# Performance work log

Hardware: AMD Instinct MI355X
Metric: run time of the kernel (lower is better)

## Reference

```python
import jax, jax.numpy as jnp
import numpy as np

B, C = 32, 32768
ENC_DIM, VOCAB, TOK_DIM, HIDDEN = 1024, 100000, 256, 512


def setup_inputs() -> dict:
    key = jax.random.key(0)
    k1, k2, k3, k4, k5 = jax.random.split(key, 5)
    enc_vec = jax.random.normal(k1, (B, ENC_DIM), dtype=jnp.float32)
    cand_tok = jax.random.randint(k2, (B, C), 0, VOCAB, dtype=jnp.int64)
    tok_emb = jax.random.normal(k3, (VOCAB, TOK_DIM), dtype=jnp.float32) * 0.02
    # PAD (0) and BOS (1) rows fixed to zeros, as in __init__
    tok_emb = tok_emb.at[0].set(0.0).at[1].set(0.0)
    W1 = jax.random.normal(k4, (HIDDEN, ENC_DIM), dtype=jnp.float32) * 0.02
    b1 = jnp.zeros((HIDDEN,), dtype=jnp.float32)
    W2 = jax.random.normal(k5, (TOK_DIM, HIDDEN), dtype=jnp.float32) * 0.02
    return {"enc_vec": enc_vec, "cand_tok": cand_tok, "tok_emb": tok_emb,
            "W1": W1, "b1": b1, "W2": W2}


def reference(enc_vec, cand_tok, tok_emb, W1, b1, W2):
    # q_proj: Linear -> GELU (exact, torch default) -> (Dropout inactive at eval) -> Linear (no bias)
    h = jax.nn.gelu(enc_vec @ W1.T + b1, approximate=False)  # (B, hidden)
    q = h @ W2.T                                             # (B, tok_dim)
    Wc = tok_emb[cand_tok]                                   # (B, C, tok_dim) gather
    logits = jnp.einsum('be,bce->bc', q, Wc)                 # (B, C)
    return logits
```

## Files before the change

kernel.cpp:

```cpp
#include <hip/hip_runtime.h>
#include <math.h>

#define B_    32
#define C_    32768
#define ENC_  1024
#define VOCAB_ 100000
#define TOK_  256
#define HID_  512

typedef __attribute__((ext_vector_type(8))) short short8;
typedef __attribute__((ext_vector_type(4))) float f32x4;

__device__ __forceinline__ float gelu_exact(float x) {
    return 0.5f * x * (1.0f + erff(x * 0.70710678118654752f));
}

__device__ __forceinline__ unsigned short f2bf(float f) {
    unsigned u = __builtin_bit_cast(unsigned, f);
    return (unsigned short)((u + 0x7fffu + ((u >> 16) & 1u)) >> 16);
}

__device__ __forceinline__ short8 pack8(float4 a, float4 b) {
    short8 r;
    r[0] = (short)f2bf(a.x); r[1] = (short)f2bf(a.y);
    r[2] = (short)f2bf(a.z); r[3] = (short)f2bf(a.w);
    r[4] = (short)f2bf(b.x); r[5] = (short)f2bf(b.y);
    r[6] = (short)f2bf(b.z); r[7] = (short)f2bf(b.w);
    return r;
}

__global__ __launch_bounds__(256) void k1_hidden(
    const float* __restrict__ enc, const float* __restrict__ W1,
    const float* __restrict__ b1, float* __restrict__ h)
{
    __shared__ float enc_lds[ENC_];
    const int b = blockIdx.y;
    const int tid = threadIdx.x;
    ((float4*)enc_lds)[tid] = ((const float4*)(enc + b * ENC_))[tid];
    __syncthreads();

    const int hw = tid >> 5, lane = tid & 31;
    const int jbase = blockIdx.x * 64 + hw * 8;
    const float4* enc4 = (const float4*)enc_lds;
    #pragma unroll
    for (int i = 0; i < 8; ++i) {
        const int j = jbase + i;
        const float4* wrow = (const float4*)(W1 + (size_t)j * ENC_);
        float acc = 0.f;
        #pragma unroll
        for (int t = 0; t < 8; ++t) {
            const int k4 = t * 32 + lane;
            float4 w = wrow[k4];
            float4 e = enc4[k4];
            acc += w.x * e.x + w.y * e.y + w.z * e.z + w.w * e.w;
        }
        #pragma unroll
        for (int m = 16; m >= 1; m >>= 1) acc += __shfl_xor(acc, m, 32);
        if (lane == 0) h[b * HID_ + j] = gelu_exact(acc + b1[j]);
    }
}

__global__ __launch_bounds__(256) void k2_q(
    const float* __restrict__ h, const float* __restrict__ W2,
    float* __restrict__ q)
{
    __shared__ float h_lds[HID_];
    const int b = blockIdx.y;
    const int tid = threadIdx.x;
    ((float2*)h_lds)[tid] = ((const float2*)(h + b * HID_))[tid];
    __syncthreads();

    const int hw = tid >> 5, lane = tid & 31;
    const int jbase = blockIdx.x * 64 + hw * 8;
    const float4* h4 = (const float4*)h_lds;
    #pragma unroll
    for (int i = 0; i < 8; ++i) {
        const int j = jbase + i;
        const float4* wrow = (const float4*)(W2 + (size_t)j * HID_);
        float acc = 0.f;
        #pragma unroll
        for (int t = 0; t < 4; ++t) {
            const int k4 = t * 32 + lane;
            float4 w = wrow[k4];
            float4 e = h4[k4];
            acc += w.x * e.x + w.y * e.y + w.z * e.z + w.w * e.w;
        }
        #pragma unroll
        for (int m = 16; m >= 1; m >>= 1) acc += __shfl_xor(acc, m, 32);
        if (lane == 0) q[b * TOK_ + j] = acc;
    }
}

__global__ __launch_bounds__(256) void k3_qall_mfma(
    const float* __restrict__ q, const float* __restrict__ tok_emb,
    float* __restrict__ q_all)
{
    __shared__ short8 q_lds[1024];
    const int tid  = threadIdx.x;
    const int lane = tid & 63;
    const int hw   = tid >> 6;
    const int m  = lane & 15;
    const int kq = lane >> 4;

    #pragma unroll
    for (int ks2 = 0; ks2 < 2; ++ks2) {
        const int ks = hw * 2 + ks2;
        #pragma unroll
        for (int n = 0; n < 2; ++n) {
            const float4* p = (const float4*)(q + (n * 16 + m) * TOK_ + ks * 32 + kq * 8);
            q_lds[(ks * 2 + n) * 64 + lane] = pack8(p[0], p[1]);
        }
    }
    __syncthreads();

    const int wave = blockIdx.x * 4 + hw;
    if (wave >= VOCAB_ / 32) return;
    const int v0 = wave * 32;

    const float* abase = tok_emb + (size_t)(v0 + m) * TOK_ + kq * 8;

    float4 st[2][4];
    #pragma unroll
    for (int t = 0; t < 2; ++t) {
        st[0][t * 2 + 0] = *(const float4*)(abase + t * 16 * TOK_);
        st[0][t * 2 + 1] = *(const float4*)(abase + t * 16 * TOK_ + 4);
    }

    f32x4 acc[2][2] = {{{0.f,0.f,0.f,0.f},{0.f,0.f,0.f,0.f}},
                       {{0.f,0.f,0.f,0.f},{0.f,0.f,0.f,0.f}}};
    #pragma unroll
    for (int ks = 0; ks < 8; ++ks) {
        const int cur = ks & 1, nxt = cur ^ 1;
        if (ks < 7) {
            #pragma unroll
            for (int t = 0; t < 2; ++t) {
                st[nxt][t * 2 + 0] = *(const float4*)(abase + t * 16 * TOK_ + (ks + 1) * 32);
                st[nxt][t * 2 + 1] = *(const float4*)(abase + t * 16 * TOK_ + (ks + 1) * 32 + 4);
            }
        }
        short8 b0 = q_lds[(ks * 2 + 0) * 64 + lane];
        short8 b1 = q_lds[(ks * 2 + 1) * 64 + lane];
        #pragma unroll
        for (int t = 0; t < 2; ++t) {
            short8 af = pack8(st[cur][t * 2 + 0], st[cur][t * 2 + 1]);
            acc[t][0] = __builtin_amdgcn_mfma_f32_16x16x32_bf16(af, b0, acc[t][0], 0, 0, 0);
            acc[t][1] = __builtin_amdgcn_mfma_f32_16x16x32_bf16(af, b1, acc[t][1], 0, 0, 0);
        }
    }

    #pragma unroll
    for (int t = 0; t < 2; ++t) {
        #pragma unroll
        for (int n = 0; n < 2; ++n) {
            float4 r;
            r.x = acc[t][n][0]; r.y = acc[t][n][1];
            r.z = acc[t][n][2]; r.w = acc[t][n][3];
            float* dst = q_all + (size_t)(n * 16 + m) * VOCAB_ + v0 + t * 16 + kq * 4;
            *(float4*)dst = r;
        }
    }
}

__global__ __launch_bounds__(256) void k4_gather(
    const int* __restrict__ cand, const float* __restrict__ q_all,
    float* __restrict__ out)
{
    const int b     = blockIdx.x & 31;
    const int chunk = blockIdx.x >> 5;
    const int c0 = chunk * 1024 + threadIdx.x * 4;
    const int4 t = *(const int4*)(cand + (size_t)b * C_ + c0);
    const float* row = q_all + (size_t)b * VOCAB_;
    float4 r;
    r.x = row[t.x];
    r.y = row[t.y];
    r.z = row[t.z];
    r.w = row[t.w];
    *(float4*)(out + (size_t)b * C_ + c0) = r;
}

extern "C" void kernel_launch(void* const* d_in, const int* in_sizes, int n_in,
                              void* d_out, int out_size, void* d_ws, size_t ws_size,
                              hipStream_t stream) {
    const float* enc     = (const float*)d_in[0];
    const int*   cand    = (const int*)  d_in[1];
    const float* tok_emb = (const float*)d_in[2];
    const float* W1      = (const float*)d_in[3];
    const float* b1      = (const float*)d_in[4];
    const float* W2      = (const float*)d_in[5];
    float* out = (float*)d_out;

    float* h     = (float*)d_ws;
    float* q     = h + B_ * HID_;
    float* q_all = q + B_ * TOK_;

    k1_hidden<<<dim3(8, 32), 256, 0, stream>>>(enc, W1, b1, h);
    k2_q     <<<dim3(4, 32), 256, 0, stream>>>(h, W2, q);

    const int tiles = VOCAB_ / 32;
    k3_qall_mfma<<<(tiles + 3) / 4, 256, 0, stream>>>(q, tok_emb, q_all);

    k4_gather<<<32 * 32, 256, 0, stream>>>(cand, q_all, out);
}
```

Before: 198.3 us.

## Store q_all as bf16 and use persistent atomic-counter tile scheduling

The q_all intermediate is now written and read as bf16, halving the traffic for the scatter-like store and the random gather. The MFMA kernel becomes a persistent grid of 512 blocks, where each wave grabs vocab tiles from a global atomic counter that is reset with a memset. This cuts the q_all footprint and its cache pressure, at the cost of an extra memset launch, per-tile atomics, and bf16 rounding on the output logits.

```diff
diff --git a/kernel.cpp b/kernel.cpp
--- a/kernel.cpp
+++ b/kernel.cpp
@@ -1,4 +1,5 @@
 #include <hip/hip_runtime.h>
+#include <hip/hip_bf16.h>
 #include <math.h>
 
 #define B_    32
@@ -7,6 +8,7 @@
 #define VOCAB_ 100000
 #define TOK_  256
 #define HID_  512
+#define TILES_ (VOCAB_ / 32)
 
 typedef __attribute__((ext_vector_type(8))) short short8;
 typedef __attribute__((ext_vector_type(4))) float f32x4;
@@ -93,7 +95,7 @@
 
 __global__ __launch_bounds__(256) void k3_qall_mfma(
     const float* __restrict__ q, const float* __restrict__ tok_emb,
-    float* __restrict__ q_all)
+    __hip_bfloat16* __restrict__ q_all, int* __restrict__ counter)
 {
     __shared__ short8 q_lds[1024];
     const int tid  = threadIdx.x;
@@ -113,68 +115,72 @@
     }
     __syncthreads();
 
-    const int wave = blockIdx.x * 4 + hw;
-    if (wave >= VOCAB_ / 32) return;
-    const int v0 = wave * 32;
-
-    const float* abase = tok_emb + (size_t)(v0 + m) * TOK_ + kq * 8;
-
-    float4 st[2][4];
-    #pragma unroll
-    for (int t = 0; t < 2; ++t) {
-        st[0][t * 2 + 0] = *(const float4*)(abase + t * 16 * TOK_);
-        st[0][t * 2 + 1] = *(const float4*)(abase + t * 16 * TOK_ + 4);
-    }
-
-    f32x4 acc[2][2] = {{{0.f,0.f,0.f,0.f},{0.f,0.f,0.f,0.f}},
-                       {{0.f,0.f,0.f,0.f},{0.f,0.f,0.f,0.f}}};
-    #pragma unroll
-    for (int ks = 0; ks < 8; ++ks) {
-        const int cur = ks & 1, nxt = cur ^ 1;
-        if (ks < 7) {
+    for (;;) {
+        int tile;
+        if (lane == 0) tile = atomicAdd(counter, 1);
+        tile = __builtin_amdgcn_readfirstlane(tile);
+        if (tile >= TILES_) break;
+        const int v0 = tile * 32;
+
+        const float* abase = tok_emb + (size_t)(v0 + m) * TOK_ + kq * 8;
+
+        float4 st[2][4];
+        #pragma unroll
+        for (int t = 0; t < 2; ++t) {
+            st[0][t * 2 + 0] = *(const float4*)(abase + t * 16 * TOK_);
+            st[0][t * 2 + 1] = *(const float4*)(abase + t * 16 * TOK_ + 4);
+        }
+
+        f32x4 acc[2][2] = {{{0.f,0.f,0.f,0.f},{0.f,0.f,0.f,0.f}},
+                           {{0.f,0.f,0.f,0.f},{0.f,0.f,0.f,0.f}}};
+        #pragma unroll
+        for (int ks = 0; ks < 8; ++ks) {
+            const int cur = ks & 1, nxt = cur ^ 1;
+            if (ks < 7) {
+                #pragma unroll
+                for (int t = 0; t < 2; ++t) {
+                    st[nxt][t * 2 + 0] = *(const float4*)(abase + t * 16 * TOK_ + (ks + 1) * 32);
+                    st[nxt][t * 2 + 1] = *(const float4*)(abase + t * 16 * TOK_ + (ks + 1) * 32 + 4);
+                }
+            }
+            short8 b0 = q_lds[(ks * 2 + 0) * 64 + lane];
+            short8 b1 = q_lds[(ks * 2 + 1) * 64 + lane];
             #pragma unroll
             for (int t = 0; t < 2; ++t) {
-                st[nxt][t * 2 + 0] = *(const float4*)(abase + t * 16 * TOK_ + (ks + 1) * 32);
-                st[nxt][t * 2 + 1] = *(const float4*)(abase + t * 16 * TOK_ + (ks + 1) * 32 + 4);
+                short8 af = pack8(st[cur][t * 2 + 0], st[cur][t * 2 + 1]);
+                acc[t][0] = __builtin_amdgcn_mfma_f32_16x16x32_bf16(af, b0, acc[t][0], 0, 0, 0);
+                acc[t][1] = __builtin_amdgcn_mfma_f32_16x16x32_bf16(af, b1, acc[t][1], 0, 0, 0);
             }
         }
-        short8 b0 = q_lds[(ks * 2 + 0) * 64 + lane];
-        short8 b1 = q_lds[(ks * 2 + 1) * 64 + lane];
+
         #pragma unroll
         for (int t = 0; t < 2; ++t) {
-            short8 af = pack8(st[cur][t * 2 + 0], st[cur][t * 2 + 1]);
-            acc[t][0] = __builtin_amdgcn_mfma_f32_16x16x32_bf16(af, b0, acc[t][0], 0, 0, 0);
-            acc[t][1] = __builtin_amdgcn_mfma_f32_16x16x32_bf16(af, b1, acc[t][1], 0, 0, 0);
-        }
-    }
-
-    #pragma unroll
-    for (int t = 0; t < 2; ++t) {
-        #pragma unroll
-        for (int n = 0; n < 2; ++n) {
-            float4 r;
-            r.x = acc[t][n][0]; r.y = acc[t][n][1];
-            r.z = acc[t][n][2]; r.w = acc[t][n][3];
-            float* dst = q_all + (size_t)(n * 16 + m) * VOCAB_ + v0 + t * 16 + kq * 4;
-            *(float4*)dst = r;
+            #pragma unroll
+            for (int n = 0; n < 2; ++n) {
+                ushort4 r;
+                r.x = f2bf(acc[t][n][0]); r.y = f2bf(acc[t][n][1]);
+                r.z = f2bf(acc[t][n][2]); r.w = f2bf(acc[t][n][3]);
+                __hip_bfloat16* dst = q_all + (size_t)(n * 16 + m) * VOCAB_ + v0 + t * 16 + kq * 4;
+                *(ushort4*)dst = r;
+            }
         }
     }
 }
 
 __global__ __launch_bounds__(256) void k4_gather(
-    const int* __restrict__ cand, const float* __restrict__ q_all,
+    const int* __restrict__ cand, const __hip_bfloat16* __restrict__ q_all,
     float* __restrict__ out)
 {
     const int b     = blockIdx.x & 31;
     const int chunk = blockIdx.x >> 5;
     const int c0 = chunk * 1024 + threadIdx.x * 4;
     const int4 t = *(const int4*)(cand + (size_t)b * C_ + c0);
-    const float* row = q_all + (size_t)b * VOCAB_;
+    const __hip_bfloat16* row = q_all + (size_t)b * VOCAB_;
     float4 r;
-    r.x = row[t.x];
-    r.y = row[t.y];
-    r.z = row[t.z];
-    r.w = row[t.w];
+    r.x = __bfloat162float(row[t.x]);
+    r.y = __bfloat162float(row[t.y]);
+    r.z = __bfloat162float(row[t.z]);
+    r.w = __bfloat162float(row[t.w]);
     *(float4*)(out + (size_t)b * C_ + c0) = r;
 }
 
@@ -189,15 +195,15 @@
     const float* W2      = (const float*)d_in[5];
     float* out = (float*)d_out;
 
-    float* h     = (float*)d_ws;
-    float* q     = h + B_ * HID_;
-    float* q_all = q + B_ * TOK_;
+    float* h = (float*)d_ws;
+    float* q = h + B_ * HID_;
+    __hip_bfloat16* q_all = (__hip_bfloat16*)(q + B_ * TOK_);
+    int* counter = (int*)((char*)(q_all + (size_t)B_ * VOCAB_) + 256);
+
+    hipMemsetAsync(counter, 0, sizeof(int), stream);
 
     k1_hidden<<<dim3(8, 32), 256, 0, stream>>>(enc, W1, b1, h);
     k2_q     <<<dim3(4, 32), 256, 0, stream>>>(h, W2, q);
-
-    const int tiles = VOCAB_ / 32;
-    k3_qall_mfma<<<(tiles + 3) / 4, 256, 0, stream>>>(q, tok_emb, q_all);
-
+    k3_qall_mfma<<<512, 256, 0, stream>>>(q, tok_emb, q_all, counter);
     k4_gather<<<32 * 32, 256, 0, stream>>>(cand, q_all, out);
 }
```

Result: slower. 230.2 us (+16.1%).
